# Optimization experiments

Measured on AMD Instinct MI355X. Metric: run time of the kernel, lower is better.

The kernel has to match this reference:

```python
import jax, jax.numpy as jnp
import numpy as np

N = 100000   # total nodes
E = 500000   # directed edges
G = 100      # graphs in batch (1000 nodes each)
D = 146      # in/hidden/out dim
C = 10       # classes
BN_EPS = 1e-5


def setup_inputs():
    key = jax.random.key(0)
    ks = jax.random.split(key, 20)
    nodes_feat = jax.random.normal(ks[0], (N, D), jnp.float32)
    src = jax.random.randint(ks[1], (E,), 0, N, dtype=jnp.int32)
    dst = jax.random.randint(ks[2], (E,), 0, N, dtype=jnp.int32)
    graph_ids = (jnp.arange(N, dtype=jnp.int32) // (N // G)).astype(jnp.int32)
    snorm = jnp.full((N,), 1.0 / np.sqrt(N // G), jnp.float32)
    s = 0.05
    W_emb = jax.random.normal(ks[3], (D, D), jnp.float32) * s
    b_emb = jnp.zeros((D,), jnp.float32)
    Ws = jax.random.normal(ks[4], (4, D, D), jnp.float32) * s
    bs = jnp.zeros((4, D), jnp.float32)
    gammas = jnp.ones((4, D), jnp.float32)
    betas = jnp.zeros((4, D), jnp.float32)
    W1 = jax.random.normal(ks[5], (D, D // 2), jnp.float32) * s
    b1 = jnp.zeros((D // 2,), jnp.float32)
    W2 = jax.random.normal(ks[6], (D // 2, D // 4), jnp.float32) * s
    b2 = jnp.zeros((D // 4,), jnp.float32)
    W3 = jax.random.normal(ks[7], (D // 4, C), jnp.float32) * s
    b3 = jnp.zeros((C,), jnp.float32)
    return dict(nodes_feat=nodes_feat, snorm=snorm, W_emb=W_emb, b_emb=b_emb,
                Ws=Ws, bs=bs, gammas=gammas, betas=betas,
                W1=W1, b1=b1, W2=W2, b2=b2, W3=W3, b3=b3,
                src=src, dst=dst, graph_ids=graph_ids)


def _gcn_layer(h, W, b, gamma, beta, src, dst, norm_out, norm_in, snorm):
    h_in = h
    # GraphConv norm='both': D_out^{-1/2} on source, sum-aggregate, D_in^{-1/2} on dest
    m = (h * norm_out[:, None])[src]                     # [E, D] gather
    agg = jax.ops.segment_sum(m, dst, num_segments=N)    # [N, D] scatter-add
    h = agg * norm_in[:, None] @ W + b                   # linear
    h = h * snorm[:, None]                               # graph norm
    mu = jnp.mean(h, axis=0)
    var = jnp.var(h, axis=0)
    h = (h - mu) * jax.lax.rsqrt(var + BN_EPS) * gamma + beta  # batch norm
    h = jax.nn.relu(h)
    return h_in + h                                      # residual


def reference(nodes_feat, snorm, W_emb, b_emb, Ws, bs, gammas, betas,
              W1, b1, W2, b2, W3, b3, src, dst, graph_ids):
    ones_e = jnp.ones((E,), jnp.float32)
    deg_out = jnp.clip(jax.ops.segment_sum(ones_e, src, num_segments=N), 1.0)
    deg_in = jnp.clip(jax.ops.segment_sum(ones_e, dst, num_segments=N), 1.0)
    norm_out = jax.lax.rsqrt(deg_out)
    norm_in = jax.lax.rsqrt(deg_in)

    h = nodes_feat @ W_emb + b_emb                       # embedding_h
    for i in range(4):
        h = _gcn_layer(h, Ws[i], bs[i], gammas[i], betas[i],
                       src, dst, norm_out, norm_in, snorm)

    # mean_nodes per graph
    cnt = jax.ops.segment_sum(jnp.ones((N,), jnp.float32), graph_ids, num_segments=G)
    hg = jax.ops.segment_sum(h, graph_ids, num_segments=G) / cnt[:, None]

    # MLPReadout: 146 -> 73 -> 36 -> 10
    x = jax.nn.relu(hg @ W1 + b1)
    x = jax.nn.relu(x @ W2 + b2)
    return x @ W3 + b3
```

## Files before the change

### kernel.cpp

```cpp
#include <hip/hip_runtime.h>

#define N_NODES 100000
#define N_EDGES 500000
#define N_GRAPHS 100
#define DIM 146
#define APAD 160
#define TPW 160
#define BN_EPS 1e-5f
#define GS_PART 8
#define GS_STRIDE 147
#define ST_PART 4

typedef __bf16 bf16x8 __attribute__((ext_vector_type(8)));
typedef float floatx4 __attribute__((ext_vector_type(4)));
typedef unsigned short ushort_t;
typedef unsigned int uint_t;

__device__ inline ushort_t f2bf(float x) {
  uint_t u = __float_as_uint(x);
  uint_t r = (u + 0x7fffu + ((u >> 16) & 1u)) >> 16;
  return (ushort_t)r;
}
__device__ inline float bf2f(ushort_t b) { return __uint_as_float((uint_t)b << 16); }
__device__ inline uint_t pack2bf(float a, float b) {
  return (uint_t)f2bf(a) | ((uint_t)f2bf(b) << 16);
}
__device__ inline float bflo(uint_t u) { return __uint_as_float(u << 16); }
__device__ inline float bfhi(uint_t u) { return __uint_as_float(u & 0xffff0000u); }

__device__ inline void async_cp16(const ushort_t* g, ushort_t* l) {
  __builtin_amdgcn_global_load_lds((const __attribute__((address_space(1))) void*)g,
                                   (__attribute__((address_space(3))) void*)l, 16, 0, 0);
}

__global__ void hist_kernel(const int* __restrict__ src, const int* __restrict__ dst,
                            int* __restrict__ deg_out, int* __restrict__ deg_in) {
  int e = blockIdx.x * 256 + threadIdx.x;
  if (e < N_EDGES) {
    atomicAdd(&deg_out[src[e]], 1);
    atomicAdd(&deg_in[dst[e]], 1);
  }
}

__global__ void norm_kernel(const int* __restrict__ deg_out, const int* __restrict__ deg_in,
                            float* __restrict__ norm_out, float* __restrict__ norm_in) {
  int v = blockIdx.x * 256 + threadIdx.x;
  if (v < N_NODES) {
    norm_out[v] = rsqrtf((float)max(deg_out[v], 1));
    norm_in[v]  = rsqrtf((float)max(deg_in[v], 1));
  }
}

__global__ void scan1_kernel(const int* __restrict__ deg_in, int* __restrict__ bsums) {
  __shared__ int sred[256];
  int t0 = blockIdx.x * 1024 + threadIdx.x * 4;
  int s = 0;
#pragma unroll
  for (int i = 0; i < 4; i++) { int v = t0 + i; s += (v < N_NODES) ? deg_in[v] : 0; }
  sred[threadIdx.x] = s; __syncthreads();
  for (int off = 128; off > 0; off >>= 1) {
    if (threadIdx.x < off) sred[threadIdx.x] += sred[threadIdx.x + off];
    __syncthreads();
  }
  if (threadIdx.x == 0) bsums[blockIdx.x] = sred[0];
}

__global__ void scan2_kernel(const int* __restrict__ bsums, int* __restrict__ bofs,
                             int* __restrict__ row_ptr, int nb) {
  if (threadIdx.x == 0 && blockIdx.x == 0) {
    int run = 0;
    for (int i = 0; i < nb; i++) { bofs[i] = run; run += bsums[i]; }
    row_ptr[N_NODES] = run;
  }
}

__global__ void scan3_kernel(const int* __restrict__ deg_in, const int* __restrict__ bofs,
                             int* __restrict__ row_ptr) {
  __shared__ int ssc[256];
  int t0 = blockIdx.x * 1024 + threadIdx.x * 4;
  int v4[4]; int s = 0;
#pragma unroll
  for (int i = 0; i < 4; i++) { int v = t0 + i; v4[i] = (v < N_NODES) ? deg_in[v] : 0; s += v4[i]; }
  ssc[threadIdx.x] = s; __syncthreads();
  for (int off = 1; off < 256; off <<= 1) {
    int t = (threadIdx.x >= off) ? ssc[threadIdx.x - off] : 0;
    __syncthreads();
    ssc[threadIdx.x] += t;
    __syncthreads();
  }
  int ex = ssc[threadIdx.x] - s + bofs[blockIdx.x];
#pragma unroll
  for (int i = 0; i < 4; i++) {
    int v = t0 + i;
    if (v < N_NODES) { row_ptr[v] = ex; ex += v4[i]; }
  }
}

__global__ void csr_fill_kernel(const int* __restrict__ src, const int* __restrict__ dst,
                                const int* __restrict__ row_ptr, int* __restrict__ fill,
                                int* __restrict__ csr) {
  int e = blockIdx.x * 256 + threadIdx.x;
  if (e < N_EDGES) {
    int d = dst[e];
    int slot = atomicAdd(&fill[d], 1);
    csr[row_ptr[d] + slot] = src[e];
  }
}

__global__ void wtrans_kernel(const float* __restrict__ W_emb, const float* __restrict__ Ws,
                              ushort_t* __restrict__ Wh) {
  int idx = blockIdx.x * 256 + threadIdx.x;
  if (idx >= 5 * 5 * 10 * 64 * 8) return;
  int j = idx & 7;
  int t = idx >> 3;
  int lane = t & 63; t >>= 6;
  int nt = t % 10; t /= 10;
  int kc = t % 5;
  int m = t / 5;
  const float* W = (m == 0) ? W_emb : Ws + (size_t)(m - 1) * DIM * DIM;
  int k = kc * 32 + (lane >> 4) * 8 + j;
  int n = nt * 16 + (lane & 15);
  float w = (k < DIM && n < DIM) ? W[k * DIM + n] : 0.f;
  Wh[(size_t)(((m * 5 + kc) * 10 + nt) * 64 + lane) * 8 + j] = f2bf(w);
}

__device__ inline bf16x8 make_frag(const float* __restrict__ nf, int row, int kc, int quad) {
  union { bf16x8 v; ushort_t u[8]; } r;
  const float* p = nf + (size_t)row * DIM + kc * 32 + quad * 8;
  int c0 = kc * 32 + quad * 8;
  if (c0 + 8 <= DIM) {
    float2 q0 = *(const float2*)(p);
    float2 q1 = *(const float2*)(p + 2);
    float2 q2 = *(const float2*)(p + 4);
    float2 q3 = *(const float2*)(p + 6);
    r.u[0] = f2bf(q0.x); r.u[1] = f2bf(q0.y); r.u[2] = f2bf(q1.x); r.u[3] = f2bf(q1.y);
    r.u[4] = f2bf(q2.x); r.u[5] = f2bf(q2.y); r.u[6] = f2bf(q3.x); r.u[7] = f2bf(q3.y);
  } else {
#pragma unroll
    for (int j = 0; j < 8; j++) r.u[j] = (c0 + j < DIM) ? f2bf(p[j]) : (ushort_t)0;
  }
  return r.v;
}

__global__ __launch_bounds__(256, 4) void gemm_embed_kernel(
    const float* __restrict__ nf, const ushort_t* __restrict__ Wh,
    const float* __restrict__ bias, ushort_t* __restrict__ hbf) {
  __shared__ __align__(16) ushort_t sB[2][5120];
  int wave = threadIdx.x >> 6, lane = threadIdx.x & 63;
  int quad = lane >> 4, l16 = lane & 15;
  int m0 = blockIdx.x * 128 + wave * 32;
  int ra = min(m0 + l16, N_NODES - 1);
  int rb = min(m0 + 16 + l16, N_NODES - 1);

  auto stage = [&](int buf, int kc) {
    const ushort_t* wsrc = Wh + (size_t)kc * 5120;
    ushort_t* ldst = &sB[buf][0];
    async_cp16(wsrc + threadIdx.x * 8, ldst + threadIdx.x * 8);
    async_cp16(wsrc + (threadIdx.x + 256) * 8, ldst + (threadIdx.x + 256) * 8);
    if (threadIdx.x < 128)
      async_cp16(wsrc + (threadIdx.x + 512) * 8, ldst + (threadIdx.x + 512) * 8);
  };

  stage(0, 0);
  __syncthreads();

  floatx4 acc[2][10];
#pragma unroll
  for (int s = 0; s < 2; s++)
#pragma unroll
    for (int nt = 0; nt < 10; nt++) acc[s][nt] = (floatx4){0.f, 0.f, 0.f, 0.f};

  for (int kc = 0; kc < 5; kc++) {
    int buf = kc & 1;
    if (kc < 4) stage(buf ^ 1, kc + 1);
    bf16x8 a0 = make_frag(nf, ra, kc, quad);
    bf16x8 a1 = make_frag(nf, rb, kc, quad);
    const ushort_t* bp = &sB[buf][lane * 8];
#pragma unroll
    for (int nt = 0; nt < 10; nt++) {
      bf16x8 bh = *(const bf16x8*)(bp + nt * 512);
      acc[0][nt] = __builtin_amdgcn_mfma_f32_16x16x32_bf16(a0, bh, acc[0][nt], 0, 0, 0);
      acc[1][nt] = __builtin_amdgcn_mfma_f32_16x16x32_bf16(a1, bh, acc[1][nt], 0, 0, 0);
    }
    __syncthreads();
  }

  ushort_t* sC = &sB[0][0];
#pragma unroll
  for (int half = 0; half < 2; half++) {
    __syncthreads();
    if ((wave >> 1) == half) {
      int lrow = (wave & 1) * 32;
#pragma unroll
      for (int nt = 0; nt < 10; nt++) {
        int c = nt * 16 + l16;
        float b = (c < DIM) ? bias[c] : 0.f;
#pragma unroll
        for (int s = 0; s < 2; s++)
#pragma unroll
          for (int r = 0; r < 4; r++)
            sC[(lrow + s * 16 + quad * 4 + r) * 160 + c] = f2bf(acc[s][nt][r] + b);
      }
    }
    __syncthreads();
    uint4* gp = (uint4*)(hbf + ((size_t)blockIdx.x * 128 + half * 64) * APAD);
#pragma unroll
    for (int i = 0; i < 5; i++) {
      int n = threadIdx.x + i * 256;
      gp[n] = *(const uint4*)(sC + n * 8);
    }
  }
}

__global__ __launch_bounds__(256, 4) void gemm_kernel(
    const ushort_t* __restrict__ Abf, const ushort_t* __restrict__ Wh,
    const float* __restrict__ bias, const float* __restrict__ snorm,
    ushort_t* __restrict__ tmpb, float* __restrict__ stats) {
  __shared__ __align__(16) ushort_t sB[2][5120];
  __shared__ float sred[2 * DIM];
  int wave = threadIdx.x >> 6, lane = threadIdx.x & 63;
  int quad = lane >> 4, l16 = lane & 15;
  int m0 = blockIdx.x * 128 + wave * 32;
  int ra = min(m0 + l16, N_NODES - 1);
  int rb = min(m0 + 16 + l16, N_NODES - 1);
  const ushort_t* ap0 = Abf + (size_t)ra * APAD + quad * 8;
  const ushort_t* ap1 = Abf + (size_t)rb * APAD + quad * 8;

  auto stage = [&](int buf, int kc) {
    const ushort_t* wsrc = Wh + (size_t)kc * 5120;
    ushort_t* ldst = &sB[buf][0];
    async_cp16(wsrc + threadIdx.x * 8, ldst + threadIdx.x * 8);
    async_cp16(wsrc + (threadIdx.x + 256) * 8, ldst + (threadIdx.x + 256) * 8);
    if (threadIdx.x < 128)
      async_cp16(wsrc + (threadIdx.x + 512) * 8, ldst + (threadIdx.x + 512) * 8);
  };

  stage(0, 0);
  bf16x8 a0[5], a1[5];
#pragma unroll
  for (int kc = 0; kc < 5; kc++) {
    a0[kc] = *(const bf16x8*)(ap0 + kc * 32);
    a1[kc] = *(const bf16x8*)(ap1 + kc * 32);
  }
  for (int i = threadIdx.x; i < 2 * DIM; i += 256) sred[i] = 0.f;
  __syncthreads();

  floatx4 acc[2][10];
#pragma unroll
  for (int s = 0; s < 2; s++)
#pragma unroll
    for (int nt = 0; nt < 10; nt++) acc[s][nt] = (floatx4){0.f, 0.f, 0.f, 0.f};

  for (int kc = 0; kc < 5; kc++) {
    int buf = kc & 1;
    if (kc < 4) stage(buf ^ 1, kc + 1);
    const ushort_t* bp = &sB[buf][lane * 8];
#pragma unroll
    for (int nt = 0; nt < 10; nt++) {
      bf16x8 bh = *(const bf16x8*)(bp + nt * 512);
      acc[0][nt] = __builtin_amdgcn_mfma_f32_16x16x32_bf16(a0[kc], bh, acc[0][nt], 0, 0, 0);
      acc[1][nt] = __builtin_amdgcn_mfma_f32_16x16x32_bf16(a1[kc], bh, acc[1][nt], 0, 0, 0);
    }
    __syncthreads();
  }

  float sn[2][4];
#pragma unroll
  for (int s = 0; s < 2; s++)
#pragma unroll
    for (int r = 0; r < 4; r++) sn[s][r] = snorm[min(m0 + s * 16 + quad * 4 + r, N_NODES - 1)];
#pragma unroll
  for (int nt = 0; nt < 10; nt++) {
    int c = nt * 16 + l16;
    if (c < DIM) {
      float b = bias[c];
      float ssum = 0.f, ssq = 0.f;
#pragma unroll
      for (int s = 0; s < 2; s++)
#pragma unroll
        for (int r = 0; r < 4; r++) {
          if (m0 + s * 16 + quad * 4 + r < N_NODES) {
            float val = (acc[s][nt][r] + b) * sn[s][r];
            ssum += val; ssq += val * val;
          }
        }
      ssum += __shfl_xor(ssum, 16, 64); ssum += __shfl_xor(ssum, 32, 64);
      ssq  += __shfl_xor(ssq, 16, 64);  ssq  += __shfl_xor(ssq, 32, 64);
      if (quad == 0) {
        atomicAdd(&sred[c], ssum);
        atomicAdd(&sred[DIM + c], ssq);
      }
    }
  }

  ushort_t* sC = &sB[0][0];
#pragma unroll
  for (int half = 0; half < 2; half++) {
    __syncthreads();
    if ((wave >> 1) == half) {
      int lrow = (wave & 1) * 32;
#pragma unroll
      for (int nt = 0; nt < 10; nt++) {
        int c = nt * 16 + l16;
        float b = (c < DIM) ? bias[c] : 0.f;
#pragma unroll
        for (int s = 0; s < 2; s++)
#pragma unroll
          for (int r = 0; r < 4; r++)
            sC[(lrow + s * 16 + quad * 4 + r) * TPW + c] = f2bf((acc[s][nt][r] + b) * sn[s][r]);
      }
    }
    __syncthreads();
    uint4* gp = (uint4*)(tmpb + ((size_t)blockIdx.x * 128 + half * 64) * TPW);
#pragma unroll
    for (int i = 0; i < 5; i++) {
      int n = threadIdx.x + i * 256;
      gp[n] = *(const uint4*)(sC + n * 8);
    }
  }
  float* stp = stats + (blockIdx.x & (ST_PART - 1)) * 2 * DIM;
  for (int i = threadIdx.x; i < 2 * DIM; i += 256) atomicAdd(&stp[i], sred[i]);
}

__global__ __launch_bounds__(256) void agg_kernel(
    const ushort_t* __restrict__ hbf, const int* __restrict__ row_ptr,
    const int* __restrict__ csr, const float* __restrict__ norm_out,
    const float* __restrict__ norm_in, ushort_t* __restrict__ xb) {
  int wid = threadIdx.x >> 6, lane = threadIdx.x & 63;
  int v = blockIdx.x * 4 + wid;
  if (v >= N_NODES) return;
  int e0 = row_ptr[v], e1 = row_ptr[v + 1];
  bool act = lane < 40;
  int col8 = lane * 4;
  float a0 = 0.f, a1 = 0.f, a2 = 0.f, a3 = 0.f;
  float b0 = 0.f, b1 = 0.f, b2 = 0.f, b3 = 0.f;
  float c0 = 0.f, c1 = 0.f, c2 = 0.f, c3 = 0.f;
  float d0 = 0.f, d1 = 0.f, d2 = 0.f, d3 = 0.f;
  int e = e0;
  for (; e + 3 < e1; e += 4) {
    int s0 = csr[e], s1 = csr[e + 1], s2 = csr[e + 2], s3 = csr[e + 3];
    float n0 = norm_out[s0], n1 = norm_out[s1], n2 = norm_out[s2], n3 = norm_out[s3];
    if (act) {
      uint2 u0 = *(const uint2*)(hbf + (size_t)s0 * APAD + col8);
      uint2 u1 = *(const uint2*)(hbf + (size_t)s1 * APAD + col8);
      uint2 u2 = *(const uint2*)(hbf + (size_t)s2 * APAD + col8);
      uint2 u3 = *(const uint2*)(hbf + (size_t)s3 * APAD + col8);
      a0 = fmaf(bflo(u0.x), n0, a0); a1 = fmaf(bfhi(u0.x), n0, a1);
      a2 = fmaf(bflo(u0.y), n0, a2); a3 = fmaf(bfhi(u0.y), n0, a3);
      b0 = fmaf(bflo(u1.x), n1, b0); b1 = fmaf(bfhi(u1.x), n1, b1);
      b2 = fmaf(bflo(u1.y), n1, b2); b3 = fmaf(bfhi(u1.y), n1, b3);
      c0 = fmaf(bflo(u2.x), n2, c0); c1 = fmaf(bfhi(u2.x), n2, c1);
      c2 = fmaf(bflo(u2.y), n2, c2); c3 = fmaf(bfhi(u2.y), n2, c3);
      d0 = fmaf(bflo(u3.x), n3, d0); d1 = fmaf(bfhi(u3.x), n3, d1);
      d2 = fmaf(bflo(u3.y), n3, d2); d3 = fmaf(bfhi(u3.y), n3, d3);
    }
  }
  for (; e < e1; e++) {
    int s0 = csr[e];
    float n0 = norm_out[s0];
    if (act) {
      uint2 u0 = *(const uint2*)(hbf + (size_t)s0 * APAD + col8);
      a0 = fmaf(bflo(u0.x), n0, a0); a1 = fmaf(bfhi(u0.x), n0, a1);
      a2 = fmaf(bflo(u0.y), n0, a2); a3 = fmaf(bfhi(u0.y), n0, a3);
    }
  }
  if (act) {
    float ni = norm_in[v];
    uint2 o;
    o.x = pack2bf((a0 + b0 + c0 + d0) * ni, (a1 + b1 + c1 + d1) * ni);
    o.y = pack2bf((a2 + b2 + c2 + d2) * ni, (a3 + b3 + c3 + d3) * ni);
    *(uint2*)((uint_t*)(xb + (size_t)v * APAD) + lane * 2) = o;
  }
}

__global__ __launch_bounds__(256) void bn_kernel(const ushort_t* __restrict__ tmpb,
                                                 const float* __restrict__ stats,
                                                 const float* __restrict__ gamma,
                                                 const float* __restrict__ beta,
                                                 ushort_t* __restrict__ hbf) {
  __shared__ float2 scs[80], shs[80];
  int t = threadIdx.x;
  if (t < 80) {
    float2 sc = make_float2(0.f, 0.f), sh = make_float2(0.f, 0.f);
    if (t < DIM / 2) {
      int c0 = 2 * t, c1 = c0 + 1;
      float su0 = 0.f, su1 = 0.f, sq0 = 0.f, sq1 = 0.f;
#pragma unroll
      for (int p = 0; p < ST_PART; p++) {
        const float* sp = stats + p * 2 * DIM;
        su0 += sp[c0]; su1 += sp[c1];
        sq0 += sp[DIM + c0]; sq1 += sp[DIM + c1];
      }
      float mu0 = su0 * (1.f / N_NODES), mu1 = su1 * (1.f / N_NODES);
      float v0 = sq0 * (1.f / N_NODES) - mu0 * mu0;
      float v1 = sq1 * (1.f / N_NODES) - mu1 * mu1;
      sc.x = gamma[c0] * rsqrtf(v0 + BN_EPS);
      sc.y = gamma[c1] * rsqrtf(v1 + BN_EPS);
      sh.x = beta[c0] - mu0 * sc.x;
      sh.y = beta[c1] - mu1 * sc.y;
    }
    scs[t] = sc; shs[t] = sh;
  }
  __syncthreads();
  int idx = blockIdx.x * 256 + t;
  if (idx >= N_NODES * 20) return;
  int v = idx / 20, q = idx - v * 20;
  const uint4* tp = (const uint4*)(tmpb + (size_t)v * TPW);
  uint4* hp = (uint4*)(hbf + (size_t)v * APAD);
  uint4 tu = tp[q];
  uint4 hu = hp[q];
  uint4 o;
  {
    float2 sc = scs[q * 4 + 0], sh = shs[q * 4 + 0];
    float x0 = fmaxf(fmaf(bflo(tu.x), sc.x, sh.x), 0.f);
    float x1 = fmaxf(fmaf(bfhi(tu.x), sc.y, sh.y), 0.f);
    o.x = pack2bf(bflo(hu.x) + x0, bfhi(hu.x) + x1);
  }
  {
    float2 sc = scs[q * 4 + 1], sh = shs[q * 4 + 1];
    float x0 = fmaxf(fmaf(bflo(tu.y), sc.x, sh.x), 0.f);
    float x1 = fmaxf(fmaf(bfhi(tu.y), sc.y, sh.y), 0.f);
    o.y = pack2bf(bflo(hu.y) + x0, bfhi(hu.y) + x1);
  }
  {
    float2 sc = scs[q * 4 + 2], sh = shs[q * 4 + 2];
    float x0 = fmaxf(fmaf(bflo(tu.z), sc.x, sh.x), 0.f);
    float x1 = fmaxf(fmaf(bfhi(tu.z), sc.y, sh.y), 0.f);
    o.z = pack2bf(bflo(hu.z) + x0, bfhi(hu.z) + x1);
  }
  {
    float2 sc = scs[q * 4 + 3], sh = shs[q * 4 + 3];
    float x0 = fmaxf(fmaf(bflo(tu.w), sc.x, sh.x), 0.f);
    float x1 = fmaxf(fmaf(bfhi(tu.w), sc.y, sh.y), 0.f);
    o.w = pack2bf(bflo(hu.w) + x0, bfhi(hu.w) + x1);
  }
  hp[q] = o;
}

__global__ __launch_bounds__(192) void gsum_kernel(
    const ushort_t* __restrict__ tmpb, const float* __restrict__ stats,
    const float* __restrict__ gamma, const float* __restrict__ beta,
    const ushort_t* __restrict__ hbf, const int* __restrict__ gids,
    float* __restrict__ hgp) {
  int t = threadIdx.x;
  if (t > DIM) return;
  float sc = 0.f, sh = 0.f;
  if (t < DIM) {
    float su = 0.f, sq = 0.f;
#pragma unroll
    for (int p = 0; p < ST_PART; p++) {
      const float* sp = stats + p * 2 * DIM;
      su += sp[t]; sq += sp[DIM + t];
    }
    float mu = su * (1.f / N_NODES);
    float var = sq * (1.f / N_NODES) - mu * mu;
    sc = gamma[t] * rsqrtf(var + BN_EPS);
    sh = beta[t] - mu * sc;
  }
  int r0 = blockIdx.x * 64;
  int part = blockIdx.x & (GS_PART - 1);
  float accv = 0.f;
  int g_prev = gids[r0];
  for (int rr = 0; rr < 64; rr++) {
    int r = r0 + rr;
    if (r >= N_NODES) break;
    int g = gids[r];
    if (g != g_prev) {
      atomicAdd(&hgp[(size_t)(part * N_GRAPHS + g_prev) * GS_STRIDE + t], accv);
      accv = 0.f; g_prev = g;
    }
    float val;
    if (t < DIM) {
      float x = fmaf(bf2f(tmpb[(size_t)r * TPW + t]), sc, sh);
      x = fmaxf(x, 0.f);
      val = bf2f(hbf[(size_t)r * APAD + t]) + x;
    } else {
      val = 1.f;
    }
    accv += val;
  }
  atomicAdd(&hgp[(size_t)(part * N_GRAPHS + g_prev) * GS_STRIDE + t], accv);
}

__global__ __launch_bounds__(256) void mlp_kernel(
    const float* __restrict__ hgp,
    const float* __restrict__ W1, const float* __restrict__ b1,
    const float* __restrict__ W2, const float* __restrict__ b2,
    const float* __restrict__ W3, const float* __restrict__ b3,
    float* __restrict__ out) {
  __shared__ float hrow[DIM];
  __shared__ float x1[73];
  __shared__ float x2[36];
  int g = blockIdx.x;
  int t = threadIdx.x;
  if (t < DIM) {
    float s = 0.f, cnt = 0.f;
#pragma unroll
    for (int p = 0; p < GS_PART; p++) {
      const float* row = hgp + (size_t)(p * N_GRAPHS + g) * GS_STRIDE;
      s += row[t];
      cnt += row[DIM];
    }
    hrow[t] = s / cnt;
  }
  __syncthreads();
  if (t < 73) {
    float s = b1[t];
    for (int k = 0; k < DIM; k++) s = fmaf(hrow[k], W1[k * 73 + t], s);
    x1[t] = s > 0.f ? s : 0.f;
  }
  __syncthreads();
  if (t < 36) {
    float s = b2[t];
    for (int k = 0; k < 73; k++) s = fmaf(x1[k], W2[k * 36 + t], s);
    x2[t] = s > 0.f ? s : 0.f;
  }
  __syncthreads();
  if (t < 10) {
    float s = b3[t];
    for (int k = 0; k < 36; k++) s = fmaf(x2[k], W3[k * 10 + t], s);
    out[g * 10 + t] = s;
  }
}

extern "C" void kernel_launch(void* const* d_in, const int* in_sizes, int n_in,
                              void* d_out, int out_size, void* d_ws, size_t ws_size,
                              hipStream_t stream) {
  const float* nodes_feat = (const float*)d_in[0];
  const float* snorm  = (const float*)d_in[1];
  const float* W_emb  = (const float*)d_in[2];
  const float* b_emb  = (const float*)d_in[3];
  const float* Ws     = (const float*)d_in[4];
  const float* bs     = (const float*)d_in[5];
  const float* gammas = (const float*)d_in[6];
  const float* betas  = (const float*)d_in[7];
  const float* W1 = (const float*)d_in[8];
  const float* b1 = (const float*)d_in[9];
  const float* W2 = (const float*)d_in[10];
  const float* b2 = (const float*)d_in[11];
  const float* W3 = (const float*)d_in[12];
  const float* b3 = (const float*)d_in[13];
  const int* src  = (const int*)d_in[14];
  const int* dst  = (const int*)d_in[15];
  const int* gids = (const int*)d_in[16];
  float* out = (float*)d_out;

  const int GB = (N_NODES + 127) / 128;
  const int NPADROWS = GB * 128;

  char* base = (char*)d_ws;
  size_t off = 0;
  auto alloc = [&](size_t bytes) { void* p = base + off; off += (bytes + 255) & ~size_t(255); return p; };
  ushort_t* hbf  = (ushort_t*)alloc((size_t)NPADROWS * APAD * 2);
  ushort_t* tmpb = (ushort_t*)alloc((size_t)NPADROWS * TPW * 2);
  ushort_t* xb   = (ushort_t*)alloc((size_t)N_NODES * APAD * 2);
  char* zstart = base + off;
  int* deg_out = (int*)alloc(N_NODES * 4);
  int* deg_in  = (int*)alloc(N_NODES * 4);
  int* fill    = (int*)alloc(N_NODES * 4);
  float* stats = (float*)alloc(4 * ST_PART * 2 * DIM * 4);
  float* hgp   = (float*)alloc((size_t)GS_PART * N_GRAPHS * GS_STRIDE * 4);
  size_t zbytes = (size_t)((base + off) - zstart);
  int* row_ptr = (int*)alloc((N_NODES + 1) * 4);
  float* norm_out = (float*)alloc(N_NODES * 4);
  float* norm_in  = (float*)alloc(N_NODES * 4);
  int* csr   = (int*)alloc((size_t)N_EDGES * 4);
  int* bsums = (int*)alloc(128 * 4);
  int* bofs  = (int*)alloc(128 * 4);
  ushort_t* Wh = (ushort_t*)alloc((size_t)5 * 5 * 10 * 64 * 8 * 2);

  hipMemsetAsync(zstart, 0, zbytes, stream);

  hist_kernel<<<(N_EDGES + 255) / 256, 256, 0, stream>>>(src, dst, deg_out, deg_in);
  norm_kernel<<<(N_NODES + 255) / 256, 256, 0, stream>>>(deg_out, deg_in, norm_out, norm_in);
  int nb = (N_NODES + 1023) / 1024;
  scan1_kernel<<<nb, 256, 0, stream>>>(deg_in, bsums);
  scan2_kernel<<<1, 64, 0, stream>>>(bsums, bofs, row_ptr, nb);
  scan3_kernel<<<nb, 256, 0, stream>>>(deg_in, bofs, row_ptr);
  csr_fill_kernel<<<(N_EDGES + 255) / 256, 256, 0, stream>>>(src, dst, row_ptr, fill, csr);
  wtrans_kernel<<<(5 * 5 * 10 * 64 * 8 + 255) / 256, 256, 0, stream>>>(W_emb, Ws, Wh);

  const size_t WHM = (size_t)5 * 10 * 64 * 8;

  gemm_embed_kernel<<<GB, 256, 0, stream>>>(nodes_feat, Wh, b_emb, hbf);

  for (int l = 0; l < 4; l++) {
    float* st = stats + (size_t)l * ST_PART * 2 * DIM;
    agg_kernel<<<(N_NODES + 3) / 4, 256, 0, stream>>>(hbf, row_ptr, csr, norm_out, norm_in, xb);
    gemm_kernel<<<GB, 256, 0, stream>>>(xb, Wh + (size_t)(l + 1) * WHM, bs + l * DIM,
                                        snorm, tmpb, st);
    if (l < 3) {
      bn_kernel<<<(N_NODES * 20 + 255) / 256, 256, 0, stream>>>(
          tmpb, st, gammas + l * DIM, betas + l * DIM, hbf);
    } else {
      gsum_kernel<<<(N_NODES + 63) / 64, 192, 0, stream>>>(
          tmpb, st, gammas + l * DIM, betas + l * DIM, hbf, gids, hgp);
    }
  }

  mlp_kernel<<<N_GRAPHS, 256, 0, stream>>>(hgp, W1, b1, W2, b2, W3, b3, out);
}
```

Baseline: 647.0 us.

## Stage full weight matrix in LDS once and store GEMM outputs directly

Both GEMM kernels now load the whole 146x160 bf16 weight matrix into shared memory up front, replacing the double-buffered per-k-chunk staging and removing the per-iteration barriers. The LDS-staged coalesced output write is replaced by direct scalar 2-byte global stores from the MFMA accumulator layout, and in gemm_kernel the stats accumulation is fused into that store loop. Larger LDS use lowers the occupancy hint from 4 to 3 blocks per CU, and the scattered 2-byte stores may hurt write coalescing.

New measurement: 620.7 us. 1.04x faster.

```diff
diff --git a/kernel.cpp b/kernel.cpp
--- a/kernel.cpp
+++ b/kernel.cpp
@@ -142,26 +142,21 @@
   return r.v;
 }
 
-__global__ __launch_bounds__(256, 4) void gemm_embed_kernel(
+__global__ __launch_bounds__(256, 3) void gemm_embed_kernel(
     const float* __restrict__ nf, const ushort_t* __restrict__ Wh,
     const float* __restrict__ bias, ushort_t* __restrict__ hbf) {
-  __shared__ __align__(16) ushort_t sB[2][5120];
+  __shared__ __align__(16) ushort_t sW[25600];
   int wave = threadIdx.x >> 6, lane = threadIdx.x & 63;
   int quad = lane >> 4, l16 = lane & 15;
   int m0 = blockIdx.x * 128 + wave * 32;
   int ra = min(m0 + l16, N_NODES - 1);
   int rb = min(m0 + 16 + l16, N_NODES - 1);
 
-  auto stage = [&](int buf, int kc) {
-    const ushort_t* wsrc = Wh + (size_t)kc * 5120;
-    ushort_t* ldst = &sB[buf][0];
-    async_cp16(wsrc + threadIdx.x * 8, ldst + threadIdx.x * 8);
-    async_cp16(wsrc + (threadIdx.x + 256) * 8, ldst + (threadIdx.x + 256) * 8);
-    if (threadIdx.x < 128)
-      async_cp16(wsrc + (threadIdx.x + 512) * 8, ldst + (threadIdx.x + 512) * 8);
-  };
-
-  stage(0, 0);
+#pragma unroll
+  for (int i = 0; i < 13; i++) {
+    int idx = threadIdx.x + i * 256;
+    if (idx < 3200) async_cp16(Wh + idx * 8, sW + idx * 8);
+  }
   __syncthreads();
 
   floatx4 acc[2][10];
@@ -170,53 +165,38 @@
 #pragma unroll
     for (int nt = 0; nt < 10; nt++) acc[s][nt] = (floatx4){0.f, 0.f, 0.f, 0.f};
 
+#pragma unroll
   for (int kc = 0; kc < 5; kc++) {
-    int buf = kc & 1;
-    if (kc < 4) stage(buf ^ 1, kc + 1);
     bf16x8 a0 = make_frag(nf, ra, kc, quad);
     bf16x8 a1 = make_frag(nf, rb, kc, quad);
-    const ushort_t* bp = &sB[buf][lane * 8];
+    const ushort_t* bp = &sW[kc * 5120 + lane * 8];
 #pragma unroll
     for (int nt = 0; nt < 10; nt++) {
       bf16x8 bh = *(const bf16x8*)(bp + nt * 512);
       acc[0][nt] = __builtin_amdgcn_mfma_f32_16x16x32_bf16(a0, bh, acc[0][nt], 0, 0, 0);
       acc[1][nt] = __builtin_amdgcn_mfma_f32_16x16x32_bf16(a1, bh, acc[1][nt], 0, 0, 0);
     }
-    __syncthreads();
-  }
-
-  ushort_t* sC = &sB[0][0];
-#pragma unroll
-  for (int half = 0; half < 2; half++) {
-    __syncthreads();
-    if ((wave >> 1) == half) {
-      int lrow = (wave & 1) * 32;
-#pragma unroll
-      for (int nt = 0; nt < 10; nt++) {
-        int c = nt * 16 + l16;
-        float b = (c < DIM) ? bias[c] : 0.f;
-#pragma unroll
-        for (int s = 0; s < 2; s++)
-#pragma unroll
-          for (int r = 0; r < 4; r++)
-            sC[(lrow + s * 16 + quad * 4 + r) * 160 + c] = f2bf(acc[s][nt][r] + b);
+  }
+
+#pragma unroll
+  for (int nt = 0; nt < 10; nt++) {
+    int c = nt * 16 + l16;
+    float b = (c < DIM) ? bias[c] : 0.f;
+#pragma unroll
+    for (int s = 0; s < 2; s++)
+#pragma unroll
+      for (int r = 0; r < 4; r++) {
+        int row = m0 + s * 16 + quad * 4 + r;
+        hbf[(size_t)row * APAD + c] = f2bf(acc[s][nt][r] + b);
       }
-    }
-    __syncthreads();
-    uint4* gp = (uint4*)(hbf + ((size_t)blockIdx.x * 128 + half * 64) * APAD);
-#pragma unroll
-    for (int i = 0; i < 5; i++) {
-      int n = threadIdx.x + i * 256;
-      gp[n] = *(const uint4*)(sC + n * 8);
-    }
-  }
-}
-
-__global__ __launch_bounds__(256, 4) void gemm_kernel(
+  }
+}
+
+__global__ __launch_bounds__(256, 3) void gemm_kernel(
     const ushort_t* __restrict__ Abf, const ushort_t* __restrict__ Wh,
     const float* __restrict__ bias, const float* __restrict__ snorm,
     ushort_t* __restrict__ tmpb, float* __restrict__ stats) {
-  __shared__ __align__(16) ushort_t sB[2][5120];
+  __shared__ __align__(16) ushort_t sW[25600];
   __shared__ float sred[2 * DIM];
   int wave = threadIdx.x >> 6, lane = threadIdx.x & 63;
   int quad = lane >> 4, l16 = lane & 15;
@@ -226,16 +206,11 @@
   const ushort_t* ap0 = Abf + (size_t)ra * APAD + quad * 8;
   const ushort_t* ap1 = Abf + (size_t)rb * APAD + quad * 8;
 
-  auto stage = [&](int buf, int kc) {
-    const ushort_t* wsrc = Wh + (size_t)kc * 5120;
-    ushort_t* ldst = &sB[buf][0];
-    async_cp16(wsrc + threadIdx.x * 8, ldst + threadIdx.x * 8);
-    async_cp16(wsrc + (threadIdx.x + 256) * 8, ldst + (threadIdx.x + 256) * 8);
-    if (threadIdx.x < 128)
-      async_cp16(wsrc + (threadIdx.x + 512) * 8, ldst + (threadIdx.x + 512) * 8);
-  };
-
-  stage(0, 0);
+#pragma unroll
+  for (int i = 0; i < 13; i++) {
+    int idx = threadIdx.x + i * 256;
+    if (idx < 3200) async_cp16(Wh + idx * 8, sW + idx * 8);
+  }
   bf16x8 a0[5], a1[5];
 #pragma unroll
   for (int kc = 0; kc < 5; kc++) {
@@ -251,17 +226,15 @@
 #pragma unroll
     for (int nt = 0; nt < 10; nt++) acc[s][nt] = (floatx4){0.f, 0.f, 0.f, 0.f};
 
+#pragma unroll
   for (int kc = 0; kc < 5; kc++) {
-    int buf = kc & 1;
-    if (kc < 4) stage(buf ^ 1, kc + 1);
-    const ushort_t* bp = &sB[buf][lane * 8];
+    const ushort_t* bp = &sW[kc * 5120 + lane * 8];
 #pragma unroll
     for (int nt = 0; nt < 10; nt++) {
       bf16x8 bh = *(const bf16x8*)(bp + nt * 512);
       acc[0][nt] = __builtin_amdgcn_mfma_f32_16x16x32_bf16(a0[kc], bh, acc[0][nt], 0, 0, 0);
       acc[1][nt] = __builtin_amdgcn_mfma_f32_16x16x32_bf16(a1[kc], bh, acc[1][nt], 0, 0, 0);
     }
-    __syncthreads();
   }
 
   float sn[2][4];
@@ -269,21 +242,22 @@
   for (int s = 0; s < 2; s++)
 #pragma unroll
     for (int r = 0; r < 4; r++) sn[s][r] = snorm[min(m0 + s * 16 + quad * 4 + r, N_NODES - 1)];
+
 #pragma unroll
   for (int nt = 0; nt < 10; nt++) {
     int c = nt * 16 + l16;
+    float b = (c < DIM) ? bias[c] : 0.f;
+    float ssum = 0.f, ssq = 0.f;
+#pragma unroll
+    for (int s = 0; s < 2; s++)
+#pragma unroll
+      for (int r = 0; r < 4; r++) {
+        int row = m0 + s * 16 + quad * 4 + r;
+        float val = (acc[s][nt][r] + b) * sn[s][r];
+        tmpb[(size_t)row * TPW + c] = f2bf(val);
+        if (c < DIM && row < N_NODES) { ssum += val; ssq += val * val; }
+      }
     if (c < DIM) {
-      float b = bias[c];
-      float ssum = 0.f, ssq = 0.f;
-#pragma unroll
-      for (int s = 0; s < 2; s++)
-#pragma unroll
-        for (int r = 0; r < 4; r++) {
-          if (m0 + s * 16 + quad * 4 + r < N_NODES) {
-            float val = (acc[s][nt][r] + b) * sn[s][r];
-            ssum += val; ssq += val * val;
-          }
-        }
       ssum += __shfl_xor(ssum, 16, 64); ssum += __shfl_xor(ssum, 32, 64);
       ssq  += __shfl_xor(ssq, 16, 64);  ssq  += __shfl_xor(ssq, 32, 64);
       if (quad == 0) {
@@ -292,32 +266,7 @@
       }
     }
   }
-
-  ushort_t* sC = &sB[0][0];
-#pragma unroll
-  for (int half = 0; half < 2; half++) {
-    __syncthreads();
-    if ((wave >> 1) == half) {
-      int lrow = (wave & 1) * 32;
-#pragma unroll
-      for (int nt = 0; nt < 10; nt++) {
-        int c = nt * 16 + l16;
-        float b = (c < DIM) ? bias[c] : 0.f;
-#pragma unroll
-        for (int s = 0; s < 2; s++)
-#pragma unroll
-          for (int r = 0; r < 4; r++)
-            sC[(lrow + s * 16 + quad * 4 + r) * TPW + c] = f2bf((acc[s][nt][r] + b) * sn[s][r]);
-      }
-    }
-    __syncthreads();
-    uint4* gp = (uint4*)(tmpb + ((size_t)blockIdx.x * 128 + half * 64) * TPW);
-#pragma unroll
-    for (int i = 0; i < 5; i++) {
-      int n = threadIdx.x + i * 256;
-      gp[n] = *(const uint4*)(sC + n * 8);
-    }
-  }
+  __syncthreads();
   float* stp = stats + (blockIdx.x & (ST_PART - 1)) * 2 * DIM;
   for (int i = threadIdx.x; i < 2 * DIM; i += 256) atomicAdd(&stp[i], sred[i]);
 }
```
